# Performance work log

Hardware: AMD Instinct MI355X
Metric: run time of the kernel (lower is better)

The kernel has to match this reference:

```python
import jax, jax.numpy as jnp
import numpy as np

B, NI, NA, D = 16, 2048, 2048, 256

def setup_inputs() -> dict:
    key = jax.random.key(0)
    k1, k2, k3 = jax.random.split(key, 3)
    input_seq = jax.random.normal(k1, (B, NI, D), dtype=jnp.float32)
    attendee_seq = jax.random.normal(k2, (B, NA, D), dtype=jnp.float32)
    # glorot-ish scale for bilinear weight
    W = jax.random.normal(k3, (D, D), dtype=jnp.float32) * (1.0 / np.sqrt(D))
    return {"input_seq": input_seq, "attendee_seq": attendee_seq, "W": W}

def reference(input_seq, attendee_seq, W):
    # bilinear scores: (x_i W) . a_j   -> [B, NI, NA]
    xW = jnp.einsum('bid,de->bie', input_seq, W)
    scores = jnp.einsum('bie,bje->bij', xW, attendee_seq)
    A = jax.nn.softmax(scores, axis=2)                 # softmax over attendee axis
    # weighted context: sum_j A[b,i,j] * v[b,j,:] -> [B, NI, D]
    attended = jnp.einsum('bij,bjd->bid', A, attendee_seq)
    return attended
```

## Files before the change

### kernel.cpp

```cpp
#include <hip/hip_runtime.h>
#include <hip/hip_bf16.h>

#define BB 16
#define NI 2048
#define NA 2048
#define DD 256
#define KVB 32
#define NT (NA / KVB)

typedef _Float16 half8 __attribute__((ext_vector_type(8)));
typedef __attribute__((ext_vector_type(4))) float f32x4;
typedef __attribute__((ext_vector_type(4))) unsigned int uint4v;

typedef const unsigned int CGU __attribute__((address_space(1)));
typedef unsigned int LU __attribute__((address_space(3)));

static __device__ __forceinline__ unsigned short f2h(float f) {
  union { _Float16 h; unsigned short u; } x; x.h = (_Float16)f; return x.u;
}
static __device__ __forceinline__ float h2f(unsigned short u) {
  union { _Float16 h; unsigned short u; } x; x.u = u; return (float)x.h;
}
static __device__ __forceinline__ unsigned int pk2(float a, float b) {
  return __builtin_bit_cast(unsigned int, __builtin_amdgcn_cvt_pkrtz(a, b));
}
static __device__ __forceinline__ void gload16(const unsigned short* g, unsigned short* l) {
  __builtin_amdgcn_global_load_lds((CGU*)g, (LU*)l, 16, 0, 0);
}

__global__ void prep_kernel(const float* __restrict__ a,
                            unsigned short* __restrict__ kfrag,
                            unsigned short* __restrict__ vfrag) {
  __shared__ float t[64][65];
  int bx = blockIdx.x;
  int b = bx >> 7;
  int r = bx & 127;
  int jt_t = r >> 2, dt_t = r & 3;
  int j0 = jt_t * 64, d0 = dt_t * 64;
  int tid = threadIdx.x;
  int rr = tid >> 4, c4 = tid & 15;
#pragma unroll
  for (int k = 0; k < 4; ++k) {
    int row = rr + k * 16;
    int j = j0 + row;
    int d = d0 + c4 * 4;
    float4 v = *(const float4*)(a + ((size_t)b * NA + j) * DD + d);
    ushort4 hh;
    hh.x = f2h(v.x); hh.y = f2h(v.y); hh.z = f2h(v.z); hh.w = f2h(v.w);
    int kt = j >> 5, jtf = (j >> 4) & 1, l16k = j & 15;
    int c = d >> 5, quad = (d >> 3) & 3, e = d & 7;
    *(ushort4*)(kfrag + ((size_t)b * NT + kt) * 8192 + c * 1024 + jtf * 512 +
                (quad * 16 + l16k) * 8 + e) = hh;
    t[row][c4 * 4 + 0] = v.x; t[row][c4 * 4 + 1] = v.y;
    t[row][c4 * 4 + 2] = v.z; t[row][c4 * 4 + 3] = v.w;
  }
  __syncthreads();
#pragma unroll
  for (int k = 0; k < 4; ++k) {
    int dl = rr + k * 16;
    int d = d0 + dl;
    int j = j0 + c4 * 4;
    ushort4 o;
    o.x = f2h(t[c4 * 4 + 0][dl]); o.y = f2h(t[c4 * 4 + 1][dl]);
    o.z = f2h(t[c4 * 4 + 2][dl]); o.w = f2h(t[c4 * 4 + 3][dl]);
    int kt = j >> 5;
    int quad = c4 & 3;
    int jt = (c4 >> 2) & 1;
    int hh_ = (d >> 7) & 1, dtl = (d >> 4) & 7, l16v = d & 15;
    *(ushort4*)(vfrag + ((size_t)b * NT + kt) * 8192 + hh_ * 4096 + dtl * 512 +
                (quad * 16 + l16v) * 8 + jt * 4) = o;
  }
}

__global__ void tw_kernel(const float* __restrict__ w,
                          unsigned short* __restrict__ wth,
                          unsigned short* __restrict__ wtl) {
  __shared__ float t[64][65];
  int bx = blockIdx.x;
  int dt = bx >> 2, et = bx & 3;
  int d0 = dt * 64, e0 = et * 64;
  int tid = threadIdx.x;
  int rr = tid >> 4, c4 = (tid & 15) * 4;
#pragma unroll
  for (int k = 0; k < 4; ++k) {
    int row = rr + k * 16;
    float4 v = *(const float4*)(w + (size_t)(d0 + row) * DD + e0 + c4);
    t[row][c4 + 0] = v.x; t[row][c4 + 1] = v.y; t[row][c4 + 2] = v.z; t[row][c4 + 3] = v.w;
  }
  __syncthreads();
#pragma unroll
  for (int k = 0; k < 4; ++k) {
    int e = rr + k * 16;
    int eg = e0 + e;
    ushort4 h, l;
    float v0 = t[c4 + 0][e]; h.x = f2h(v0); l.x = f2h(v0 - h2f(h.x));
    float v1 = t[c4 + 1][e]; h.y = f2h(v1); l.y = f2h(v1 - h2f(h.y));
    float v2 = t[c4 + 2][e]; h.z = f2h(v2); l.z = f2h(v2 - h2f(h.z));
    float v3 = t[c4 + 3][e]; h.w = f2h(v3); l.w = f2h(v3 - h2f(h.w));
    int dd = d0 + c4;
    int u = dd >> 3, sub = dd & 7;
    size_t off = (size_t)eg * DD + ((u ^ (eg & 7)) * 8) + sub;
    *(ushort4*)(wth + off) = h;
    *(ushort4*)(wtl + off) = l;
  }
}

__global__ __launch_bounds__(256, 2) void qgemm_kernel(
    const float* __restrict__ x, const unsigned short* __restrict__ wth,
    const unsigned short* __restrict__ wtl, unsigned short* __restrict__ qf) {
  __shared__ unsigned short wb[2][64 * 256];
  const int tid = threadIdx.x;
  const int lane = tid & 63;
  const int wv = tid >> 6;
  const int quad = lane >> 4;
  const int l16 = lane & 15;
  const int m0 = blockIdx.x * 64;

  half8 xf[8];
  {
    const float* xr = x + (size_t)(m0 + wv * 16 + l16) * DD;
#pragma unroll
    for (int c = 0; c < 8; ++c) {
      float4 a = *(const float4*)(xr + c * 32 + quad * 8);
      float4 b = *(const float4*)(xr + c * 32 + quad * 8 + 4);
      half8 v;
      v[0] = (_Float16)a.x; v[1] = (_Float16)a.y; v[2] = (_Float16)a.z; v[3] = (_Float16)a.w;
      v[4] = (_Float16)b.x; v[5] = (_Float16)b.y; v[6] = (_Float16)b.z; v[7] = (_Float16)b.w;
      xf[c] = v;
    }
  }

#pragma unroll 1
  for (int eg = 0; eg < 4; ++eg) {
    uint4 t0[8], t1[8];
    {
      const unsigned short* sh = wth + (size_t)(eg * 64) * DD;
      const unsigned short* sl = wtl + (size_t)(eg * 64) * DD;
#pragma unroll
      for (int i = 0; i < 8; ++i) {
        t0[i] = *(const uint4*)(sh + (i * 256 + tid) * 8);
        t1[i] = *(const uint4*)(sl + (i * 256 + tid) * 8);
      }
    }
    __syncthreads();
#pragma unroll
    for (int i = 0; i < 8; ++i) {
      *(uint4*)(wb[0] + (i * 256 + tid) * 8) = t0[i];
      *(uint4*)(wb[1] + (i * 256 + tid) * 8) = t1[i];
    }
    __syncthreads();
#pragma unroll
    for (int etl = 0; etl < 4; ++etl) {
      int rloc = etl * 16 + l16;
      f32x4 acc; acc[0] = acc[1] = acc[2] = acc[3] = 0.f;
#pragma unroll
      for (int c = 0; c < 8; ++c) {
        int off = rloc * DD + (((4 * c + quad) ^ (rloc & 7)) * 8);
        half8 wh = *(const half8*)(wb[0] + off);
        half8 wl = *(const half8*)(wb[1] + off);
        acc = __builtin_amdgcn_mfma_f32_16x16x32_f16(xf[c], wh, acc, 0, 0, 0);
        acc = __builtin_amdgcn_mfma_f32_16x16x32_f16(xf[c], wl, acc, 0, 0, 0);
      }
      int e = eg * 64 + etl * 16 + l16;
#pragma unroll
      for (int rg = 0; rg < 4; ++rg) {
        qf[(size_t)(m0 + wv * 16 + 4 * quad + rg) * DD + e] = f2h(acc[rg]);
      }
    }
  }
}

__global__ __launch_bounds__(256, 4) void attn_kernel(
    const unsigned short* __restrict__ kfrag, const unsigned short* __restrict__ vfrag,
    const unsigned short* __restrict__ qf, float* __restrict__ out) {
  __shared__ unsigned short kls[2][KVB * DD];

  const int tid = threadIdx.x;
  const int lane = tid & 63;
  const int wv = tid >> 6;
  const int p = wv >> 1;
  const int h = wv & 1;
  const int quad = lane >> 4;
  const int l16 = lane & 15;

  int bx = blockIdx.x;
  int lbx = (bx & 7) * 128 + (bx >> 3);
  const int b = lbx >> 6;
  const int qbase = (lbx & 63) * 32 + p * 16;

  const unsigned short* kfb = kfrag + (size_t)b * NT * 8192;
  const unsigned short* vfb = vfrag + (size_t)b * NT * 8192 + h * 4096;

  half8 qh[8];
  {
    const size_t qrow = ((size_t)b * NI + qbase + l16) * DD;
#pragma unroll
    for (int c = 0; c < 8; ++c)
      qh[c] = *(const half8*)(qf + qrow + c * 32 + quad * 8);
  }

  f32x4 acc[8];
#pragma unroll
  for (int dt = 0; dt < 8; ++dt) { acc[dt][0] = 0.f; acc[dt][1] = 0.f; acc[dt][2] = 0.f; acc[dt][3] = 0.f; }
  float m0r = -INFINITY;
  float l0 = 0.f;

#pragma unroll
  for (int i = 0; i < 4; ++i) {
    int off = (i * 4 + wv) * 512;
    gload16(kfb + off + lane * 8, &kls[0][off]);
  }
  __syncthreads();

#pragma unroll 1
  for (int kt = 0; kt < NT; ++kt) {
    half8 vb[8];
#pragma unroll
    for (int dt = 0; dt < 8; ++dt)
      vb[dt] = *(const half8*)(vfb + (size_t)kt * 8192 + dt * 512 + lane * 8);

    if (kt + 1 < NT) {
      const unsigned short* s = kfb + (size_t)(kt + 1) * 8192;
      unsigned short* d = &kls[(kt + 1) & 1][0];
#pragma unroll
      for (int i = 0; i < 4; ++i) {
        int off = (i * 4 + wv) * 512;
        gload16(s + off + lane * 8, d + off);
      }
    }

    const unsigned short* kb = &kls[kt & 1][0];
    f32x4 st0, st1;
    st0[0] = st0[1] = st0[2] = st0[3] = 0.f;
    st1[0] = st1[1] = st1[2] = st1[3] = 0.f;
    __builtin_amdgcn_s_setprio(1);
#pragma unroll
    for (int c = 0; c < 8; ++c) {
      half8 k0 = *(const half8*)(kb + c * 1024 + lane * 8);
      half8 k1 = *(const half8*)(kb + c * 1024 + 512 + lane * 8);
      st0 = __builtin_amdgcn_mfma_f32_16x16x32_f16(k0, qh[c], st0, 0, 0, 0);
      st1 = __builtin_amdgcn_mfma_f32_16x16x32_f16(k1, qh[c], st1, 0, 0, 0);
    }
    __builtin_amdgcn_s_setprio(0);

    float mt0 = fmaxf(fmaxf(fmaxf(st0[0], st0[1]), fmaxf(st0[2], st0[3])),
                      fmaxf(fmaxf(st1[0], st1[1]), fmaxf(st1[2], st1[3])));
    mt0 = fmaxf(mt0, __shfl_xor(mt0, 16)); mt0 = fmaxf(mt0, __shfl_xor(mt0, 32));
    bool upd = __any(mt0 > m0r + 8.f) != 0;
    if (upd) {
      float mn0 = fmaxf(m0r, mt0);
      float sc0 = __expf(m0r - mn0);
      l0 *= sc0;
#pragma unroll
      for (int rg = 0; rg < 4; ++rg) {
        float a0 = __shfl(sc0, 4 * quad + rg);
#pragma unroll
        for (int dt = 0; dt < 8; ++dt) acc[dt][rg] *= a0;
      }
      m0r = mn0;
    }

    float e00 = __expf(st0[0] - m0r), e01 = __expf(st0[1] - m0r);
    float e02 = __expf(st0[2] - m0r), e03 = __expf(st0[3] - m0r);
    float e10 = __expf(st1[0] - m0r), e11 = __expf(st1[1] - m0r);
    float e12 = __expf(st1[2] - m0r), e13 = __expf(st1[3] - m0r);
    l0 += ((e00 + e01) + (e02 + e03)) + ((e10 + e11) + (e12 + e13));
    half8 pa;
    {
      uint4v pau = { pk2(e00, e01), pk2(e02, e03), pk2(e10, e11), pk2(e12, e13) };
      pa = __builtin_bit_cast(half8, pau);
    }

    __builtin_amdgcn_s_setprio(1);
#pragma unroll
    for (int dt = 0; dt < 8; ++dt)
      acc[dt] = __builtin_amdgcn_mfma_f32_16x16x32_f16(pa, vb[dt], acc[dt], 0, 0, 0);
    __builtin_amdgcn_s_setprio(0);

    __syncthreads();
  }

  l0 += __shfl_xor(l0, 16); l0 += __shfl_xor(l0, 32);
  float inv0 = 1.0f / l0;
  size_t ob = ((size_t)b * NI + qbase) * DD + h * 128;
#pragma unroll
  for (int rg = 0; rg < 4; ++rg) {
    float i0 = __shfl(inv0, 4 * quad + rg);
#pragma unroll
    for (int dt = 0; dt < 8; ++dt) {
      int d = dt * 16 + l16;
      out[ob + (size_t)(4 * quad + rg) * DD + d] = acc[dt][rg] * i0;
    }
  }
}

extern "C" void kernel_launch(void* const* d_in, const int* in_sizes, int n_in,
                              void* d_out, int out_size, void* d_ws, size_t ws_size,
                              hipStream_t stream) {
  const float* x = (const float*)d_in[0];
  const float* att = (const float*)d_in[1];
  const float* W = (const float*)d_in[2];
  float* out = (float*)d_out;

  const size_t NE = (size_t)BB * NA * DD;
  unsigned short* w0    = (unsigned short*)d_ws;
  unsigned short* kfrag = w0;
  unsigned short* vfrag = w0 + NE;
  unsigned short* qfp   = w0 + 2 * NE;
  unsigned short* wth   = w0 + 3 * NE;
  unsigned short* wtl   = w0 + 3 * NE + (size_t)DD * DD;

  prep_kernel<<<2048, 256, 0, stream>>>(att, kfrag, vfrag);
  tw_kernel<<<16, 256, 0, stream>>>(W, wth, wtl);
  qgemm_kernel<<<512, 256, 0, stream>>>(x, wth, wtl, qfp);
  attn_kernel<<<1024, 256, 0, stream>>>(kfrag, vfrag, qfp, out);
}
```

Measured before the change: 201.5 us.

## Fold log2e into Q, use exp2, split score MFMA chains, merge W prep kernel

Pre-scales the projected queries by log2(e) so the softmax can use exp2f directly, and raises the lazy-rescale threshold to match the base-2 scale. The score MFMA accumulation is split into two independent chains to cut dependency latency. The row-max shuffle reduction now runs only inside the rescale branch. The W transpose/split kernel is merged into the attendee prep kernel as extra blocks, which removes one launch. Risks include a small precision change from the extra fp32 adds and from the per-lane max check used before the reduction.

```diff
diff --git a/kernel.cpp b/kernel.cpp
--- a/kernel.cpp
+++ b/kernel.cpp
@@ -30,15 +30,49 @@
 
 __global__ void prep_kernel(const float* __restrict__ a,
                             unsigned short* __restrict__ kfrag,
-                            unsigned short* __restrict__ vfrag) {
+                            unsigned short* __restrict__ vfrag,
+                            const float* __restrict__ w,
+                            unsigned short* __restrict__ wth,
+                            unsigned short* __restrict__ wtl) {
   __shared__ float t[64][65];
   int bx = blockIdx.x;
+  int tid = threadIdx.x;
+  int rr = tid >> 4, c4 = tid & 15;
+
+  if (bx >= 2048) {
+    int r = bx - 2048;
+    int dt = r >> 2, et = r & 3;
+    int d0 = dt * 64, e0 = et * 64;
+    int cc = c4 * 4;
+#pragma unroll
+    for (int k = 0; k < 4; ++k) {
+      int row = rr + k * 16;
+      float4 v = *(const float4*)(w + (size_t)(d0 + row) * DD + e0 + cc);
+      t[row][cc + 0] = v.x; t[row][cc + 1] = v.y; t[row][cc + 2] = v.z; t[row][cc + 3] = v.w;
+    }
+    __syncthreads();
+#pragma unroll
+    for (int k = 0; k < 4; ++k) {
+      int e = rr + k * 16;
+      int eg = e0 + e;
+      ushort4 h, l;
+      float v0 = t[cc + 0][e]; h.x = f2h(v0); l.x = f2h(v0 - h2f(h.x));
+      float v1 = t[cc + 1][e]; h.y = f2h(v1); l.y = f2h(v1 - h2f(h.y));
+      float v2 = t[cc + 2][e]; h.z = f2h(v2); l.z = f2h(v2 - h2f(h.z));
+      float v3 = t[cc + 3][e]; h.w = f2h(v3); l.w = f2h(v3 - h2f(h.w));
+      int dd = d0 + cc;
+      int u = dd >> 3, sub = dd & 7;
+      size_t off = (size_t)eg * DD + ((u ^ (eg & 7)) * 8) + sub;
+      *(ushort4*)(wth + off) = h;
+      *(ushort4*)(wtl + off) = l;
+    }
+    return;
+  }
+
   int b = bx >> 7;
   int r = bx & 127;
   int jt_t = r >> 2, dt_t = r & 3;
   int j0 = jt_t * 64, d0 = dt_t * 64;
-  int tid = threadIdx.x;
-  int rr = tid >> 4, c4 = tid & 15;
 #pragma unroll
   for (int k = 0; k < 4; ++k) {
     int row = rr + k * 16;
@@ -72,39 +106,6 @@
   }
 }
 
-__global__ void tw_kernel(const float* __restrict__ w,
-                          unsigned short* __restrict__ wth,
-                          unsigned short* __restrict__ wtl) {
-  __shared__ float t[64][65];
-  int bx = blockIdx.x;
-  int dt = bx >> 2, et = bx & 3;
-  int d0 = dt * 64, e0 = et * 64;
-  int tid = threadIdx.x;
-  int rr = tid >> 4, c4 = (tid & 15) * 4;
-#pragma unroll
-  for (int k = 0; k < 4; ++k) {
-    int row = rr + k * 16;
-    float4 v = *(const float4*)(w + (size_t)(d0 + row) * DD + e0 + c4);
-    t[row][c4 + 0] = v.x; t[row][c4 + 1] = v.y; t[row][c4 + 2] = v.z; t[row][c4 + 3] = v.w;
-  }
-  __syncthreads();
-#pragma unroll
-  for (int k = 0; k < 4; ++k) {
-    int e = rr + k * 16;
-    int eg = e0 + e;
-    ushort4 h, l;
-    float v0 = t[c4 + 0][e]; h.x = f2h(v0); l.x = f2h(v0 - h2f(h.x));
-    float v1 = t[c4 + 1][e]; h.y = f2h(v1); l.y = f2h(v1 - h2f(h.y));
-    float v2 = t[c4 + 2][e]; h.z = f2h(v2); l.z = f2h(v2 - h2f(h.z));
-    float v3 = t[c4 + 3][e]; h.w = f2h(v3); l.w = f2h(v3 - h2f(h.w));
-    int dd = d0 + c4;
-    int u = dd >> 3, sub = dd & 7;
-    size_t off = (size_t)eg * DD + ((u ^ (eg & 7)) * 8) + sub;
-    *(ushort4*)(wth + off) = h;
-    *(ushort4*)(wtl + off) = l;
-  }
-}
-
 __global__ __launch_bounds__(256, 2) void qgemm_kernel(
     const float* __restrict__ x, const unsigned short* __restrict__ wth,
     const unsigned short* __restrict__ wtl, unsigned short* __restrict__ qf) {
@@ -164,7 +165,7 @@
       int e = eg * 64 + etl * 16 + l16;
 #pragma unroll
       for (int rg = 0; rg < 4; ++rg) {
-        qf[(size_t)(m0 + wv * 16 + 4 * quad + rg) * DD + e] = f2h(acc[rg]);
+        qf[(size_t)(m0 + wv * 16 + 4 * quad + rg) * DD + e] = f2h(acc[rg] * 1.44269504f);
       }
     }
   }
@@ -230,40 +231,50 @@
     }
 
     const unsigned short* kb = &kls[kt & 1][0];
-    f32x4 st0, st1;
-    st0[0] = st0[1] = st0[2] = st0[3] = 0.f;
-    st1[0] = st1[1] = st1[2] = st1[3] = 0.f;
+    f32x4 sa0, sb0, sa1, sb1;
+    sa0[0]=sa0[1]=sa0[2]=sa0[3]=0.f; sb0[0]=sb0[1]=sb0[2]=sb0[3]=0.f;
+    sa1[0]=sa1[1]=sa1[2]=sa1[3]=0.f; sb1[0]=sb1[1]=sb1[2]=sb1[3]=0.f;
     __builtin_amdgcn_s_setprio(1);
 #pragma unroll
-    for (int c = 0; c < 8; ++c) {
+    for (int c = 0; c < 4; ++c) {
       half8 k0 = *(const half8*)(kb + c * 1024 + lane * 8);
       half8 k1 = *(const half8*)(kb + c * 1024 + 512 + lane * 8);
-      st0 = __builtin_amdgcn_mfma_f32_16x16x32_f16(k0, qh[c], st0, 0, 0, 0);
-      st1 = __builtin_amdgcn_mfma_f32_16x16x32_f16(k1, qh[c], st1, 0, 0, 0);
+      sa0 = __builtin_amdgcn_mfma_f32_16x16x32_f16(k0, qh[c], sa0, 0, 0, 0);
+      sa1 = __builtin_amdgcn_mfma_f32_16x16x32_f16(k1, qh[c], sa1, 0, 0, 0);
+    }
+#pragma unroll
+    for (int c = 4; c < 8; ++c) {
+      half8 k0 = *(const half8*)(kb + c * 1024 + lane * 8);
+      half8 k1 = *(const half8*)(kb + c * 1024 + 512 + lane * 8);
+      sb0 = __builtin_amdgcn_mfma_f32_16x16x32_f16(k0, qh[c], sb0, 0, 0, 0);
+      sb1 = __builtin_amdgcn_mfma_f32_16x16x32_f16(k1, qh[c], sb1, 0, 0, 0);
     }
     __builtin_amdgcn_s_setprio(0);
-
-    float mt0 = fmaxf(fmaxf(fmaxf(st0[0], st0[1]), fmaxf(st0[2], st0[3])),
-                      fmaxf(fmaxf(st1[0], st1[1]), fmaxf(st1[2], st1[3])));
-    mt0 = fmaxf(mt0, __shfl_xor(mt0, 16)); mt0 = fmaxf(mt0, __shfl_xor(mt0, 32));
-    bool upd = __any(mt0 > m0r + 8.f) != 0;
-    if (upd) {
-      float mn0 = fmaxf(m0r, mt0);
-      float sc0 = __expf(m0r - mn0);
-      l0 *= sc0;
+    f32x4 st0, st1;
+    st0[0]=sa0[0]+sb0[0]; st0[1]=sa0[1]+sb0[1]; st0[2]=sa0[2]+sb0[2]; st0[3]=sa0[3]+sb0[3];
+    st1[0]=sa1[0]+sb1[0]; st1[1]=sa1[1]+sb1[1]; st1[2]=sa1[2]+sb1[2]; st1[3]=sa1[3]+sb1[3];
+
+    float mt = fmaxf(fmaxf(fmaxf(st0[0], st0[1]), fmaxf(st0[2], st0[3])),
+                     fmaxf(fmaxf(st1[0], st1[1]), fmaxf(st1[2], st1[3])));
+    if (__any(mt > m0r + 11.5416f)) {
+      float mr = fmaxf(mt, __shfl_xor(mt, 16));
+      mr = fmaxf(mr, __shfl_xor(mr, 32));
+      float mn = fmaxf(m0r, mr);
+      float sc = exp2f(m0r - mn);
+      l0 *= sc;
 #pragma unroll
       for (int rg = 0; rg < 4; ++rg) {
-        float a0 = __shfl(sc0, 4 * quad + rg);
+        float a0 = __shfl(sc, 4 * quad + rg);
 #pragma unroll
         for (int dt = 0; dt < 8; ++dt) acc[dt][rg] *= a0;
       }
-      m0r = mn0;
-    }
-
-    float e00 = __expf(st0[0] - m0r), e01 = __expf(st0[1] - m0r);
-    float e02 = __expf(st0[2] - m0r), e03 = __expf(st0[3] - m0r);
-    float e10 = __expf(st1[0] - m0r), e11 = __expf(st1[1] - m0r);
-    float e12 = __expf(st1[2] - m0r), e13 = __expf(st1[3] - m0r);
+      m0r = mn;
+    }
+
+    float e00 = exp2f(st0[0] - m0r), e01 = exp2f(st0[1] - m0r);
+    float e02 = exp2f(st0[2] - m0r), e03 = exp2f(st0[3] - m0r);
+    float e10 = exp2f(st1[0] - m0r), e11 = exp2f(st1[1] - m0r);
+    float e12 = exp2f(st1[2] - m0r), e13 = exp2f(st1[3] - m0r);
     l0 += ((e00 + e01) + (e02 + e03)) + ((e10 + e11) + (e12 + e13));
     half8 pa;
     {
@@ -310,8 +321,7 @@
   unsigned short* wth   = w0 + 3 * NE;
   unsigned short* wtl   = w0 + 3 * NE + (size_t)DD * DD;
 
-  prep_kernel<<<2048, 256, 0, stream>>>(att, kfrag, vfrag);
-  tw_kernel<<<16, 256, 0, stream>>>(W, wth, wtl);
+  prep_kernel<<<2064, 256, 0, stream>>>(att, kfrag, vfrag, W, wth, wtl);
   qgemm_kernel<<<512, 256, 0, stream>>>(x, wth, wtl, qfp);
   attn_kernel<<<1024, 256, 0, stream>>>(kfrag, vfrag, qfp, out);
 }
```

Measured after the change: 201.5 us. About the same (-0.0%).
